# Optimization experiments

Measured on AMD Instinct MI355X. Metric: run time of the kernel, lower is better.

Reference implementation:

```python
import jax, jax.numpy as jnp
import numpy as np

HIDDEN = 1024
H = 16        # num query heads
HKV = 4       # num kv heads
GROUPS = H // HKV
D = HIDDEN // H  # head_dim = 64
SW = (63, 0)  # sliding_window (left, right)
W = SW[0] + SW[1] + 1  # window length per query = 64
MAXPOS = 2048


def _sincos_table(num_pos, dim):
    # faithful to create_sinusoidal_positions (incl. final [:, :, :num_pos] slice)
    inv_freq = 1.0 / 10000 ** (np.arange(0, dim, 2, dtype=np.int32) / dim)
    freqs = np.einsum('i,j->ij', np.arange(num_pos, dtype=np.int32), inv_freq).astype(np.float32)
    emb = np.concatenate((freqs, freqs), axis=-1)
    out = np.concatenate((np.sin(emb)[:, None, :], np.cos(emb)[:, None, :]), axis=-1)
    return jnp.asarray(out[:, :, :num_pos])  # [num_pos, 1, 2*dim]

_SINCOS = _sincos_table(MAXPOS, D)


def _rotate_half(x):
    h = x.shape[-1] // 2
    return jnp.concatenate((-x[..., h:], x[..., :h]), axis=-1)


def setup_inputs() -> dict:
    key = jax.random.key(0)
    k0, k1, k2, k3, k4 = jax.random.split(key, 5)
    B, S = 1, 2048
    std = 0.02
    return {
        'hidden_states': jax.random.normal(k0, (B, S, HIDDEN), dtype=jnp.float32),
        'attention_mask': jnp.ones((B, S, 1, W), dtype=jnp.int32),
        'position_ids': jnp.arange(B * S, dtype=jnp.int32).reshape(B, S) % MAXPOS,
        'q_kernel': jax.random.normal(k1, (HIDDEN, H * D), dtype=jnp.float32) * std,
        'k_kernel': jax.random.normal(k2, (HIDDEN, HKV * D), dtype=jnp.float32) * std,
        'v_kernel': jax.random.normal(k3, (HIDDEN, HKV * D), dtype=jnp.float32) * std,
        'o_kernel': jax.random.normal(k4, (HIDDEN, HIDDEN), dtype=jnp.float32) * std,
    }


def reference(hidden_states, attention_mask, position_ids, q_kernel, k_kernel, v_kernel, o_kernel):
    B, S, _ = hidden_states.shape
    # QKV projections (no bias)
    q = (hidden_states @ q_kernel).reshape(B, S, H, D)
    k = (hidden_states @ k_kernel).reshape(B, S, HKV, D)
    v = (hidden_states @ v_kernel).reshape(B, S, HKV, D)
    # rotary embedding; sincos[pos] -> [B,S,1,2D], broadcasts over head axis
    sc = _SINCOS[position_ids]
    sin, cos = jnp.split(sc, 2, axis=-1)
    k = k * cos + _rotate_half(k) * sin
    q = q * cos + _rotate_half(q) * sin
    # GQA: repeat kv heads to match query heads
    k = jnp.repeat(k, GROUPS, axis=2)  # [B,S,H,D]
    v = jnp.repeat(v, GROUPS, axis=2)
    # sliding-window gather: each query position sees W surrounding keys
    k = jnp.pad(k, ((0, 0), SW, (0, 0), (0, 0)))
    v = jnp.pad(v, ((0, 0), SW, (0, 0), (0, 0)))
    idx = jnp.arange(W, dtype=jnp.int32)[None, :] + jnp.arange(S, dtype=jnp.int32)[:, None]  # [S,W]
    kg = k[:, idx]  # [B,S,W,H,D]
    vg = v[:, idx]
    # attention (q_len=1 per position), scores [B,S,H,W]
    scores = jnp.einsum('bshd,bswhd->bshw', q, kg) / jnp.asarray(np.sqrt(D), scores_dtype := jnp.float32)
    neg = jnp.finfo(jnp.float32).min
    m = attention_mask[:, :, 0, :][:, :, None, :]  # [B,S,1,W] broadcast over H
    bias = jnp.where(m > 0, jnp.float32(0.0), neg)
    weights = jax.nn.softmax(scores + bias, axis=-1)
    attn = jnp.einsum('bshw,bswhd->bshd', weights, vg).reshape(B, S, HIDDEN)
    return attn @ o_kernel
```

## Files before the change

### kernel.cpp

```cpp
#include <hip/hip_runtime.h>
#include <hip/hip_bf16.h>
#include <math.h>

#define S        2048
#define HIDDEN   1024
#define NH       16
#define NKV      4
#define HD       64
#define NQKV     1536
#define VW       2128

typedef _Float16 f16x8 __attribute__((ext_vector_type(8)));
typedef _Float16 f16x4 __attribute__((ext_vector_type(4)));
typedef float    f32x4 __attribute__((ext_vector_type(4)));

__device__ __forceinline__ void glds16(const void* g, void* l) {
    __builtin_amdgcn_global_load_lds((const __attribute__((address_space(1))) void*)g,
                                     (__attribute__((address_space(3))) void*)l, 16, 0, 0);
}

__device__ __host__ __forceinline__ int ropePerm(int d) {
    int t = d & 48;
    return (t == 16 || t == 32) ? (d ^ 48) : d;
}

__global__ __launch_bounds__(256) void prep_kernel(const float* __restrict__ hs, _Float16* __restrict__ hsf16,
                                                   const float* __restrict__ wq, const float* __restrict__ wk,
                                                   const float* __restrict__ wvv, const float* __restrict__ wo,
                                                   _Float16* __restrict__ wqkvT, _Float16* __restrict__ woT,
                                                   const int* __restrict__ pos_ids, float2* __restrict__ rope_tab,
                                                   _Float16* __restrict__ vTs) {
    int bid = blockIdx.x;
    int tid = threadIdx.x;
    if (bid >= 4864) {
        int d = bid - 4864;
        if (tid < 64) vTs[(size_t)d * VW + tid] = (_Float16)0.0f;
        return;
    }
    if (bid >= 4608) {
        int idx = (bid - 4608) * 256 + tid;
        int s = idx >> 5, f = idx & 31;
        double inv = pow(10000.0, -(double)(2 * f) / 64.0);
        float ang = (float)((double)pos_ids[s] * inv);
        float sn, cs;
        sincosf(ang, &sn, &cs);
        rope_tab[idx] = make_float2(sn, cs);
        return;
    }
    if (bid >= 2560) {
        int i = (bid - 2560) * 256 + tid;
        float4 v = ((const float4*)hs)[i];
        f16x4 o = { (_Float16)v.x, (_Float16)v.y, (_Float16)v.z, (_Float16)v.w };
        *(f16x4*)(hsf16 + 4 * (size_t)i) = o;
        return;
    }
    const float* src; _Float16* dst; int Cn, b; bool prm;
    if (bid < 1024)      { src = wq;  dst = wqkvT;                       Cn = 1024; b = bid;        prm = true;  }
    else if (bid < 1280) { src = wk;  dst = wqkvT + (size_t)1024 * 1024; Cn = 256;  b = bid - 1024; prm = true;  }
    else if (bid < 1536) { src = wvv; dst = wqkvT + (size_t)1280 * 1024; Cn = 256;  b = bid - 1280; prm = false; }
    else                 { src = wo;  dst = woT;                         Cn = 1024; b = bid - 1536; prm = false; }
    int xb = Cn >> 5;
    int c0 = (b % xb) * 32;
    int r0 = (b / xb) * 32;
    __shared__ float t[32][33];
    int tx = tid & 31, ty = tid >> 5;
#pragma unroll
    for (int i = ty; i < 32; i += 8)
        t[i][tx] = src[(size_t)(r0 + i) * Cn + c0 + tx];
    __syncthreads();
#pragma unroll
    for (int i = ty; i < 32; i += 8) {
        int n = c0 + i;
        int np = prm ? ((n & ~63) | ropePerm(n & 63)) : n;
        dst[(size_t)np * 1024 + r0 + tx] = (_Float16)t[tx][i];
    }
}

#define GEMM_BODY(Aptr, Bptr)                                                                   \
    f32x4 acc[2][2] = {};                                                                       \
    for (int k0 = 0; k0 < 1024; k0 += 128) {                                                    \
        __syncthreads();                                                                        \
        _Pragma("unroll")                                                                       \
        for (int u = 0; u < 4; ++u) {                                                           \
            int r = wv * 16 + u * 4 + dr;                                                       \
            glds16(Aptr + (size_t)(m0 + r) * 1024 + k0 + ((cc ^ (r & 15)) * 8),                 \
                   As + (wv * 16 + u * 4) * 128);                                               \
            glds16(Bptr + (size_t)(n0 + r) * 1024 + k0 + ((cc ^ (r & 15)) * 8),                 \
                   Bs + (wv * 16 + u * 4) * 128);                                               \
        }                                                                                       \
        __syncthreads();                                                                        \
        _Pragma("unroll")                                                                       \
        for (int ks = 0; ks < 4; ++ks) {                                                        \
            f16x8 a[2], b[2];                                                                   \
            _Pragma("unroll")                                                                   \
            for (int i = 0; i < 2; ++i) {                                                       \
                int row = wm + i * 16 + lr;                                                     \
                a[i] = *(const f16x8*)&As[row * 128 + (((ks * 4 + quad) ^ (row & 15)) * 8)];    \
            }                                                                                   \
            _Pragma("unroll")                                                                   \
            for (int j = 0; j < 2; ++j) {                                                       \
                int row = wn + j * 16 + lr;                                                     \
                b[j] = *(const f16x8*)&Bs[row * 128 + (((ks * 4 + quad) ^ (row & 15)) * 8)];    \
            }                                                                                   \
            _Pragma("unroll")                                                                   \
            for (int i = 0; i < 2; ++i)                                                         \
                _Pragma("unroll")                                                               \
                for (int j = 0; j < 2; ++j)                                                     \
                    acc[i][j] = __builtin_amdgcn_mfma_f32_16x16x32_f16(a[i], b[j], acc[i][j], 0, 0, 0); \
        }                                                                                       \
    }

__global__ __launch_bounds__(256) void gemm_qkv(const _Float16* __restrict__ A,
                                                const _Float16* __restrict__ BT,
                                                _Float16* __restrict__ qkv,
                                                _Float16* __restrict__ vTs,
                                                const float2* __restrict__ rope_tab) {
    __shared__ __align__(16) _Float16 As[64 * 128];
    __shared__ __align__(16) _Float16 Bs[64 * 128];
    const int bid  = blockIdx.x;
    const int tid  = threadIdx.x;
    const int lane = tid & 63;
    const int wv   = tid >> 6;
    const int lr   = lane & 15;
    const int quad = lane >> 4;
    const int dr   = lane >> 4;
    const int cc   = lane & 15;
    const int wm   = (wv >> 1) * 32;
    const int wn   = (wv & 1) * 32;
    const int bx = bid % 24, by = bid / 24;
    const int m0 = by * 64, n0 = bx * 64;

    GEMM_BODY(A, BT)

    if (n0 < 1280) {
        const bool isq = (n0 < 1024);
        const int  f   = (wn >> 1) + lr;
#pragma unroll
        for (int i = 0; i < 2; ++i)
#pragma unroll
            for (int r = 0; r < 4; ++r) {
                int s = m0 + wm + i * 16 + quad * 4 + r;
                float2 scv = rope_tab[(size_t)s * 32 + f];
                float lo = acc[i][0][r], hi = acc[i][1][r];
                float nlo = lo * scv.y - hi * scv.x;
                float nhi = hi * scv.y + lo * scv.x;
                if (isq) { nlo *= 0.125f; nhi *= 0.125f; }
                qkv[(size_t)s * NQKV + n0 + wn + lr]      = (_Float16)nlo;
                qkv[(size_t)s * NQKV + n0 + wn + 16 + lr] = (_Float16)nhi;
            }
    } else {
#pragma unroll
        for (int i = 0; i < 2; ++i)
#pragma unroll
            for (int j = 0; j < 2; ++j) {
                int d = n0 - 1280 + wn + j * 16 + lr;
                f16x4 h = { (_Float16)acc[i][j][0], (_Float16)acc[i][j][1],
                            (_Float16)acc[i][j][2], (_Float16)acc[i][j][3] };
                *(f16x4*)(vTs + (size_t)d * VW + 64 + m0 + wm + i * 16 + quad * 4) = h;
            }
    }
}

__global__ __launch_bounds__(256) void gemm_o(const _Float16* __restrict__ A,
                                              const _Float16* __restrict__ BT,
                                              float* __restrict__ out) {
    __shared__ __align__(16) _Float16 As[64 * 128];
    __shared__ __align__(16) _Float16 Bs[64 * 128];
    const int bid  = blockIdx.x;
    const int tid  = threadIdx.x;
    const int lane = tid & 63;
    const int wv   = tid >> 6;
    const int lr   = lane & 15;
    const int quad = lane >> 4;
    const int dr   = lane >> 4;
    const int cc   = lane & 15;
    const int wm   = (wv >> 1) * 32;
    const int wn   = (wv & 1) * 32;
    const int bx = bid % 16, by = bid / 16;
    const int m0 = by * 64, n0 = bx * 64;

    GEMM_BODY(A, BT)

#pragma unroll
    for (int i = 0; i < 2; ++i)
#pragma unroll
        for (int j = 0; j < 2; ++j)
#pragma unroll
            for (int r = 0; r < 4; ++r)
                out[(size_t)(m0 + wm + i * 16 + quad * 4 + r) * 1024 + n0 + wn + j * 16 + lr] = acc[i][j][r];
}

__global__ __launch_bounds__(256) void attn_mfma(const _Float16* __restrict__ qkv,
                                                 const _Float16* __restrict__ vTs,
                                                 const int* __restrict__ mask,
                                                 _Float16* __restrict__ attn_out) {
    const int s0   = blockIdx.x * 16;
    const int g    = blockIdx.y;
    const int tid  = threadIdx.x;
    const int lane = tid & 63;
    const int wv   = tid >> 6;
    const int h    = g * 4 + wv;
    const int lr   = lane & 15;
    const int quad = lane >> 4;

    __shared__ __align__(16) _Float16 K_lds[80 * 72];
    __shared__ __align__(16) _Float16 Vt_lds[64 * 104];
    __shared__ __align__(16) _Float16 P_lds[4][16 * 104];
    __shared__ int M_lds[1024];

    ((int4*)M_lds)[tid] = ((const int4*)(mask + s0 * 64))[tid];

    for (int c = tid; c < 640; c += 256) {
        int r = c >> 3, cl = c & 7;
        int j = s0 - 64 + r;
        f16x8 val = {};
        if (j >= 0)
            val = *(const f16x8*)(qkv + (size_t)j * NQKV + 1024 + g * 64 + cl * 8);
        *(f16x8*)&K_lds[r * 72 + cl * 8] = val;
    }
    for (int c = tid; c < 64 * 12; c += 256) {
        int d = c / 12, ch = c % 12;
        *(f16x8*)&Vt_lds[d * 104 + ch * 8] =
            *(const f16x8*)(vTs + (size_t)(g * 64 + d) * VW + s0 + ch * 8);
    }
    f16x8 qf[2];
#pragma unroll
    for (int ks = 0; ks < 2; ++ks)
        qf[ks] = *(const f16x8*)(qkv + (size_t)(s0 + lr) * NQKV + h * 64 + ks * 32 + quad * 8);
    __syncthreads();

    f32x4 sc[5];
#pragma unroll
    for (int t = 0; t < 5; ++t) {
        f32x4 a = {};
#pragma unroll
        for (int ks = 0; ks < 2; ++ks) {
            f16x8 kf = *(const f16x8*)&K_lds[(t * 16 + lr) * 72 + ks * 32 + quad * 8];
            a = __builtin_amdgcn_mfma_f32_16x16x32_f16(qf[ks], kf, a, 0, 0, 0);
        }
        sc[t] = a;
    }
#pragma unroll
    for (int t = 0; t < 5; ++t)
#pragma unroll
        for (int r = 0; r < 4; ++r) {
            int qi = quad * 4 + r;
            int w  = t * 16 + lr - 1 - qi;
            bool ok = (w >= 0) && (w < 64) && (M_lds[qi * 64 + (w & 63)] > 0);
            sc[t][r] = ok ? sc[t][r] : -1e30f;
        }
    float pr[5][4];
#pragma unroll
    for (int r = 0; r < 4; ++r) {
        float mx = -1e30f;
#pragma unroll
        for (int t = 0; t < 5; ++t) mx = fmaxf(mx, sc[t][r]);
#pragma unroll
        for (int off = 1; off < 16; off <<= 1) mx = fmaxf(mx, __shfl_xor(mx, off));
        float sum = 0.f;
#pragma unroll
        for (int t = 0; t < 5; ++t) { float e = __expf(sc[t][r] - mx); pr[t][r] = e; sum += e; }
#pragma unroll
        for (int off = 1; off < 16; off <<= 1) sum += __shfl_xor(sum, off);
        float rs = 1.0f / sum;
#pragma unroll
        for (int t = 0; t < 5; ++t) pr[t][r] *= rs;
    }
    _Float16* myP = P_lds[wv];
    {
        f16x4 z = {};
        *(f16x4*)&myP[lr * 104 + 80 + quad * 4] = z;
    }
#pragma unroll
    for (int t = 0; t < 5; ++t)
#pragma unroll
        for (int r = 0; r < 4; ++r)
            myP[(quad * 4 + r) * 104 + t * 16 + lr] = (_Float16)pr[t][r];
    __syncthreads();

    f32x4 oacc[4] = {};
#pragma unroll
    for (int ks = 0; ks < 3; ++ks) {
        f16x8 pf = *(const f16x8*)&myP[lr * 104 + ks * 32 + quad * 8];
#pragma unroll
        for (int t = 0; t < 4; ++t) {
            f16x8 vf = *(const f16x8*)&Vt_lds[(t * 16 + lr) * 104 + ks * 32 + quad * 8];
            oacc[t] = __builtin_amdgcn_mfma_f32_16x16x32_f16(pf, vf, oacc[t], 0, 0, 0);
        }
    }
#pragma unroll
    for (int t = 0; t < 4; ++t)
#pragma unroll
        for (int r = 0; r < 4; ++r)
            attn_out[(size_t)(s0 + quad * 4 + r) * HIDDEN + h * 64 + t * 16 + lr] = (_Float16)oacc[t][r];
}

extern "C" void kernel_launch(void* const* d_in, const int* in_sizes, int n_in,
                              void* d_out, int out_size, void* d_ws, size_t ws_size,
                              hipStream_t stream) {
    const float* hs      = (const float*)d_in[0];
    const int*   mask    = (const int*)  d_in[1];
    const int*   pos_ids = (const int*)  d_in[2];
    const float* wq      = (const float*)d_in[3];
    const float* wk      = (const float*)d_in[4];
    const float* wvv     = (const float*)d_in[5];
    const float* wo      = (const float*)d_in[6];
    float* out = (float*)d_out;

    char* ws = (char*)d_ws;
    _Float16* wqkvT   = (_Float16*)(ws + 0);
    _Float16* woT     = (_Float16*)(ws + (3u << 20));
    _Float16* hsf16   = (_Float16*)(ws + (5u << 20));
    _Float16* qkvf16  = (_Float16*)(ws + (9u << 20));
    _Float16* attnf16 = (_Float16*)(ws + (15u << 20));
    _Float16* vTs     = (_Float16*)(ws + (19u << 20));
    float2*   ropeTab = (float2*)  (ws + (21u << 20));

    prep_kernel<<<5120, 256, 0, stream>>>(hs, hsf16, wq, wk, wvv, wo, wqkvT, woT,
                                          pos_ids, ropeTab, vTs);
    gemm_qkv<<<768, 256, 0, stream>>>(hsf16, wqkvT, qkvf16, vTs, ropeTab);
    attn_mfma<<<dim3(S / 16, NKV), 256, 0, stream>>>(qkvf16, vTs, mask, attnf16);
    gemm_o<<<512, 256, 0, stream>>>(attnf16, woT, out);
}
```

Before: 107.6 us.

## Double-buffer GEMM LDS tiles to overlap global loads with MFMA compute

The shared GEMM body for the QKV and output projections now splits K into 64-wide stages and ping-pongs between two LDS buffers. The next stage's global-to-LDS loads are issued before MFMA work on the current buffer, and each iteration needs one barrier instead of two. The swizzle and the per-lane load mapping are adjusted for the narrower 64-column tile, so total LDS use stays the same. The trade-off is twice as many loop iterations and barriers per K sweep. If the compiler adds conservative vmcnt waits before the LDS reads, the intended overlap may be lost.

```diff
diff --git a/kernel.cpp b/kernel.cpp
--- a/kernel.cpp
+++ b/kernel.cpp
@@ -76,31 +76,35 @@
     }
 }
 
+#define GEMM_STAGE(Aptr, Bptr, k0, buf)                                                         \
+    _Pragma("unroll")                                                                           \
+    for (int u = 0; u < 2; ++u) {                                                               \
+        int r = wv * 16 + u * 8 + dr;                                                           \
+        glds16(Aptr + (size_t)(m0 + r) * 1024 + (k0) + ((cc ^ (r & 7)) * 8),                    \
+               &As[buf][(wv * 16 + u * 8) * 64]);                                               \
+        glds16(Bptr + (size_t)(n0 + r) * 1024 + (k0) + ((cc ^ (r & 7)) * 8),                    \
+               &Bs[buf][(wv * 16 + u * 8) * 64]);                                               \
+    }
+
 #define GEMM_BODY(Aptr, Bptr)                                                                   \
     f32x4 acc[2][2] = {};                                                                       \
-    for (int k0 = 0; k0 < 1024; k0 += 128) {                                                    \
+    GEMM_STAGE(Aptr, Bptr, 0, 0)                                                                \
+    int p = 0;                                                                                  \
+    for (int it = 0; it < 16; ++it) {                                                           \
         __syncthreads();                                                                        \
+        if (it < 15) { GEMM_STAGE(Aptr, Bptr, (it + 1) * 64, p ^ 1) }                           \
         _Pragma("unroll")                                                                       \
-        for (int u = 0; u < 4; ++u) {                                                           \
-            int r = wv * 16 + u * 4 + dr;                                                       \
-            glds16(Aptr + (size_t)(m0 + r) * 1024 + k0 + ((cc ^ (r & 15)) * 8),                 \
-                   As + (wv * 16 + u * 4) * 128);                                               \
-            glds16(Bptr + (size_t)(n0 + r) * 1024 + k0 + ((cc ^ (r & 15)) * 8),                 \
-                   Bs + (wv * 16 + u * 4) * 128);                                               \
-        }                                                                                       \
-        __syncthreads();                                                                        \
-        _Pragma("unroll")                                                                       \
-        for (int ks = 0; ks < 4; ++ks) {                                                        \
+        for (int ks = 0; ks < 2; ++ks) {                                                        \
             f16x8 a[2], b[2];                                                                   \
             _Pragma("unroll")                                                                   \
             for (int i = 0; i < 2; ++i) {                                                       \
                 int row = wm + i * 16 + lr;                                                     \
-                a[i] = *(const f16x8*)&As[row * 128 + (((ks * 4 + quad) ^ (row & 15)) * 8)];    \
+                a[i] = *(const f16x8*)&As[p][row * 64 + (((ks * 4 + quad) ^ (row & 7)) * 8)];   \
             }                                                                                   \
             _Pragma("unroll")                                                                   \
             for (int j = 0; j < 2; ++j) {                                                       \
                 int row = wn + j * 16 + lr;                                                     \
-                b[j] = *(const f16x8*)&Bs[row * 128 + (((ks * 4 + quad) ^ (row & 15)) * 8)];    \
+                b[j] = *(const f16x8*)&Bs[p][row * 64 + (((ks * 4 + quad) ^ (row & 7)) * 8)];   \
             }                                                                                   \
             _Pragma("unroll")                                                                   \
             for (int i = 0; i < 2; ++i)                                                         \
@@ -108,6 +112,7 @@
                 for (int j = 0; j < 2; ++j)                                                     \
                     acc[i][j] = __builtin_amdgcn_mfma_f32_16x16x32_f16(a[i], b[j], acc[i][j], 0, 0, 0); \
         }                                                                                       \
+        p ^= 1;                                                                                 \
     }
 
 __global__ __launch_bounds__(256) void gemm_qkv(const _Float16* __restrict__ A,
@@ -115,16 +120,16 @@
                                                 _Float16* __restrict__ qkv,
                                                 _Float16* __restrict__ vTs,
                                                 const float2* __restrict__ rope_tab) {
-    __shared__ __align__(16) _Float16 As[64 * 128];
-    __shared__ __align__(16) _Float16 Bs[64 * 128];
+    __shared__ __align__(16) _Float16 As[2][64 * 64];
+    __shared__ __align__(16) _Float16 Bs[2][64 * 64];
     const int bid  = blockIdx.x;
     const int tid  = threadIdx.x;
     const int lane = tid & 63;
     const int wv   = tid >> 6;
     const int lr   = lane & 15;
     const int quad = lane >> 4;
-    const int dr   = lane >> 4;
-    const int cc   = lane & 15;
+    const int dr   = lane >> 3;
+    const int cc   = lane & 7;
     const int wm   = (wv >> 1) * 32;
     const int wn   = (wv & 1) * 32;
     const int bx = bid % 24, by = bid / 24;
@@ -164,16 +169,16 @@
 __global__ __launch_bounds__(256) void gemm_o(const _Float16* __restrict__ A,
                                               const _Float16* __restrict__ BT,
                                               float* __restrict__ out) {
-    __shared__ __align__(16) _Float16 As[64 * 128];
-    __shared__ __align__(16) _Float16 Bs[64 * 128];
+    __shared__ __align__(16) _Float16 As[2][64 * 64];
+    __shared__ __align__(16) _Float16 Bs[2][64 * 64];
     const int bid  = blockIdx.x;
     const int tid  = threadIdx.x;
     const int lane = tid & 63;
     const int wv   = tid >> 6;
     const int lr   = lane & 15;
     const int quad = lane >> 4;
-    const int dr   = lane >> 4;
-    const int cc   = lane & 15;
+    const int dr   = lane >> 3;
+    const int cc   = lane & 7;
     const int wm   = (wv >> 1) * 32;
     const int wn   = (wv & 1) * 32;
     const int bx = bid % 16, by = bid / 16;
```

After: 118.3 us. 1.1x slower.
